# Kernel optimization log

Hardware: AMD Instinct MI355X
Metric: run time of the kernel (lower is better)

## Reference

```python
import jax, jax.numpy as jnp
import numpy as np

NUM_HEADS = 12

def setup_inputs() -> dict:
    key = jax.random.key(0)
    ks = jax.random.split(key, 9)
    B, N, C = 4, 1024, 768
    hd = C // NUM_HEADS  # 64
    return {
        "x": jax.random.normal(ks[0], (B, N, C), dtype=jnp.float32),
        "prev_attn": jax.random.uniform(ks[1], (B, NUM_HEADS, N, N), dtype=jnp.float32) / N,
        "qkv_w": jax.random.normal(ks[2], (3 * C, C), dtype=jnp.float32) * 0.02,
        "proj_w": jax.random.normal(ks[3], (C, C), dtype=jnp.float32) * 0.02,
        "proj_b": jax.random.normal(ks[4], (C,), dtype=jnp.float32) * 0.02,
        "bp_w1": jax.random.normal(ks[5], (hd // 2, 2 * hd), dtype=jnp.float32) * 0.02,
        "bp_b1": jax.random.normal(ks[6], (hd // 2,), dtype=jnp.float32) * 0.02,
        "bp_w2": jax.random.normal(ks[7], (3, hd // 2), dtype=jnp.float32) * 0.02,
        "bp_b2": jax.random.normal(ks[8], (3,), dtype=jnp.float32) * 0.02,
    }

def reference(x, prev_attn, qkv_w, proj_w, proj_b, bp_w1, bp_b1, bp_w2, bp_b2):
    B, N, C = x.shape
    H = NUM_HEADS
    hd = C // H
    scale = hd ** -0.5
    # qkv projection: [B,N,3C] -> [3,B,H,N,hd]
    qkv = (x @ qkv_w.T).reshape(B, N, 3, H, hd).transpose(2, 0, 3, 1, 4)
    q, k, v = qkv[0], qkv[1], qkv[2]
    # scaled dot-product scores [B,H,N,N]
    attn_logits = jnp.einsum('bhnd,bhmd->bhnm', q, k) * scale
    cur_attn = jax.nn.softmax(attn_logits, axis=-1)
    # per-(b,h,n) bias MLP on concat(q,k): [B,H,N,2*hd] -> [B,H,N,3]
    qk = jnp.concatenate((q, k), axis=-1)
    h1 = jax.nn.relu(jnp.einsum('bhnd,od->bhno', qk, bp_w1) + bp_b1)
    bias = jnp.abs(jnp.einsum('bhno,po->bhnp', h1, bp_w2) + bp_b2)  # [B,H,N,3]
    # blend current attention, previous attention, and uniform term
    attn = (cur_attn * (1.0 + bias[..., 0:1])
            + prev_attn * bias[..., 1:2]
            - bias[..., 2:3] / N)
    out = jnp.einsum('bhnm,bhmd->bhnd', attn, v)  # [B,H,N,hd]
    out = out.transpose(0, 2, 1, 3).reshape(B, N, C)
    out = out @ proj_w.T + proj_b
    return (out, cur_attn)
```

## Files before the change

### kernel.cpp

```cpp
#include <hip/hip_runtime.h>

typedef __bf16 bf16_t;
typedef __bf16 bf16x8 __attribute__((ext_vector_type(8)));
typedef __bf16 bf16x4 __attribute__((ext_vector_type(4)));
typedef float f32x4 __attribute__((ext_vector_type(4)));

static constexpr int Bb = 4, Hh = 12, Nn = 1024, Cc = 768, HD = 64;
static constexpr int OUT0 = Bb * Nn * Cc;

__global__ __launch_bounds__(256) void convert_all(
    const float* __restrict__ x, const float* __restrict__ qw, const float* __restrict__ pw,
    bf16_t* __restrict__ xb, bf16_t* __restrict__ qwb, bf16_t* __restrict__ pwb) {
  const int NX = (Bb * Nn * Cc) / 4;
  const int NQ = (3 * Cc * Cc) / 4;
  int i = blockIdx.x * 256 + threadIdx.x;
  const float4* src;
  bf16_t* dst;
  int off;
  if (i < NX) { src = (const float4*)x; dst = xb; off = i; }
  else if (i < NX + NQ) { src = (const float4*)qw; dst = qwb; off = i - NX; }
  else { src = (const float4*)pw; dst = pwb; off = i - NX - NQ; }
  float4 v = src[off];
  bf16x4 o;
  o[0] = (bf16_t)v.x; o[1] = (bf16_t)v.y; o[2] = (bf16_t)v.z; o[3] = (bf16_t)v.w;
  *(bf16x4*)(dst + (size_t)off * 4) = o;
}

template <int MODE>
__global__ __launch_bounds__(256) void gemm_bt(
    const bf16_t* __restrict__ A, const bf16_t* __restrict__ Bm, int N, int K,
    bf16_t* __restrict__ q_bf, bf16_t* __restrict__ k_bf, bf16_t* __restrict__ vT_bf,
    float* __restrict__ outF, const float* __restrict__ bias) {
  __shared__ bf16_t As[128 * 40];
  __shared__ bf16_t Bs[128 * 40];
  const int tid = threadIdx.x;
  const int lane = tid & 63;
  const int w = tid >> 6;
  const int wr = w >> 1, wc = w & 1;
  const int g = lane >> 4, r = lane & 15;
  const int ntiles = N >> 7;
  const int m0 = (blockIdx.x / ntiles) << 7;
  const int n0 = (blockIdx.x % ntiles) << 7;

  const f32x4 fz = {0.f, 0.f, 0.f, 0.f};
  f32x4 acc[4][4];
#pragma unroll
  for (int i = 0; i < 4; i++)
#pragma unroll
    for (int j = 0; j < 4; j++) acc[i][j] = fz;

  for (int k0 = 0; k0 < K; k0 += 32) {
#pragma unroll
    for (int p = 0; p < 2; p++) {
      int idx = tid + (p << 8);
      int row = idx >> 2;
      int kof = (idx & 3) << 3;
      *(bf16x8*)&As[row * 40 + kof] = *(const bf16x8*)&A[(size_t)(m0 + row) * K + k0 + kof];
      *(bf16x8*)&Bs[row * 40 + kof] = *(const bf16x8*)&Bm[(size_t)(n0 + row) * K + k0 + kof];
    }
    __syncthreads();
    bf16x8 af[4], bfv[4];
#pragma unroll
    for (int i = 0; i < 4; i++) af[i] = *(const bf16x8*)&As[(wr * 64 + i * 16 + r) * 40 + g * 8];
#pragma unroll
    for (int j = 0; j < 4; j++) bfv[j] = *(const bf16x8*)&Bs[(wc * 64 + j * 16 + r) * 40 + g * 8];
#pragma unroll
    for (int i = 0; i < 4; i++)
#pragma unroll
      for (int j = 0; j < 4; j++)
        acc[i][j] = __builtin_amdgcn_mfma_f32_16x16x32_bf16(af[i], bfv[j], acc[i][j], 0, 0, 0);
    __syncthreads();
  }

#pragma unroll
  for (int i = 0; i < 4; i++) {
#pragma unroll
    for (int j = 0; j < 4; j++) {
      int c = n0 + wc * 64 + j * 16 + r;
#pragma unroll
      for (int e = 0; e < 4; e++) {
        int mrow = m0 + wr * 64 + i * 16 + g * 4 + e;
        float val = acc[i][j][e];
        if constexpr (MODE == 0) {
          int which = c / 768;
          int cc = c - which * 768;
          int h = cc >> 6, d = cc & 63;
          int b = mrow >> 10, n = mrow & 1023;
          size_t bh = (size_t)(b * Hh + h);
          if (which == 0)      q_bf[(bh * Nn + n) * HD + d] = (bf16_t)val;
          else if (which == 1) k_bf[(bh * Nn + n) * HD + d] = (bf16_t)val;
          else                 vT_bf[(bh * HD + d) * Nn + n] = (bf16_t)val;
        } else {
          outF[(size_t)mrow * N + c] = val + bias[c];
        }
      }
    }
  }
}

__global__ __launch_bounds__(256) void bias_mlp(
    const bf16_t* __restrict__ qb, const bf16_t* __restrict__ kb,
    const float* __restrict__ w1, const float* __restrict__ b1,
    const float* __restrict__ w2, const float* __restrict__ b2,
    float* __restrict__ bias4) {
  __shared__ float w1s[32 * 129];
  __shared__ float qks[8][128];
  __shared__ float h1s[8][32];
  const int t = threadIdx.x;
#pragma unroll
  for (int p = 0; p < 16; p++) {
    int idx = p * 256 + t;
    w1s[(idx >> 7) * 129 + (idx & 127)] = w1[idx];
  }
  const int rl = t >> 5, u = t & 31;
  const int rowg = blockIdx.x * 8 + rl;
  {
    int i4 = u * 4;
    const bf16_t* src = (i4 < 64) ? (qb + (size_t)rowg * HD + i4)
                                  : (kb + (size_t)rowg * HD + (i4 - 64));
    bf16x4 vv = *(const bf16x4*)src;
#pragma unroll
    for (int z = 0; z < 4; z++) qks[rl][i4 + z] = (float)vv[z];
  }
  __syncthreads();
  float accv = b1[u];
#pragma unroll 8
  for (int i = 0; i < 128; i++) accv += qks[rl][i] * w1s[u * 129 + i];
  h1s[rl][u] = fmaxf(accv, 0.f);
  __syncthreads();
  if (u < 4) {
    float outv = 0.f;
    if (u < 3) {
      float s = b2[u];
#pragma unroll
      for (int j = 0; j < 32; j++) s += w2[u * 32 + j] * h1s[rl][j];
      float v = fabsf(s);
      outv = (u == 0) ? (1.f + v) : ((u == 1) ? v : -v * (1.f / (float)Nn));
    }
    bias4[(size_t)rowg * 4 + u] = outv;
  }
}

__global__ __launch_bounds__(256) void attn_fused(
    const bf16_t* __restrict__ qb, const bf16_t* __restrict__ kb,
    const bf16_t* __restrict__ vT, const float* __restrict__ prev,
    const float* __restrict__ bias4, float* __restrict__ cur,
    bf16_t* __restrict__ oh) {
  __shared__ bf16_t Pb[16 * 1024];
  __shared__ float redmax[16][4];
  __shared__ float redsum[16][4];
  const int bid = blockIdx.x;
  const int bh = bid >> 6, mt = bid & 63;
  const int tid = threadIdx.x;
  const int lane = tid & 63, w = tid >> 6;
  const int g = lane >> 4, r = lane & 15;
  const int row0 = mt << 4;

  const bf16_t* qp = qb + ((size_t)bh * Nn + row0) * HD;
  const bf16_t* kp = kb + (size_t)bh * Nn * HD;
  bf16x8 a0 = *(const bf16x8*)&qp[r * HD + g * 8];
  bf16x8 a1 = *(const bf16x8*)&qp[r * HD + g * 8 + 32];
  const f32x4 fz = {0.f, 0.f, 0.f, 0.f};
  f32x4 acc[16];
#pragma unroll
  for (int t = 0; t < 16; t++) {
    int col = (w << 8) + (t << 4) + r;
    bf16x8 b0 = *(const bf16x8*)&kp[(size_t)col * HD + g * 8];
    bf16x8 b1 = *(const bf16x8*)&kp[(size_t)col * HD + g * 8 + 32];
    f32x4 z = __builtin_amdgcn_mfma_f32_16x16x32_bf16(a0, b0, fz, 0, 0, 0);
    acc[t] = __builtin_amdgcn_mfma_f32_16x16x32_bf16(a1, b1, z, 0, 0, 0);
  }
  const float scale = 0.125f;
  float mj[4] = {-3.0e38f, -3.0e38f, -3.0e38f, -3.0e38f};
#pragma unroll
  for (int t = 0; t < 16; t++)
#pragma unroll
    for (int e = 0; e < 4; e++) {
      acc[t][e] *= scale;
      mj[e] = fmaxf(mj[e], acc[t][e]);
    }
#pragma unroll
  for (int s = 1; s < 16; s <<= 1)
#pragma unroll
    for (int e = 0; e < 4; e++) mj[e] = fmaxf(mj[e], __shfl_xor(mj[e], s, 64));
  if (r == 0) {
#pragma unroll
    for (int e = 0; e < 4; e++) redmax[g * 4 + e][w] = mj[e];
  }
  __syncthreads();
  float rm[4];
#pragma unroll
  for (int e = 0; e < 4; e++) {
    float v = fmaxf(redmax[g * 4 + e][0], redmax[g * 4 + e][1]);
    rm[e] = fmaxf(v, fmaxf(redmax[g * 4 + e][2], redmax[g * 4 + e][3]));
  }
  float sj[4] = {0.f, 0.f, 0.f, 0.f};
#pragma unroll
  for (int t = 0; t < 16; t++)
#pragma unroll
    for (int e = 0; e < 4; e++) {
      float ev = __expf(acc[t][e] - rm[e]);
      acc[t][e] = ev;
      sj[e] += ev;
    }
#pragma unroll
  for (int s = 1; s < 16; s <<= 1)
#pragma unroll
    for (int e = 0; e < 4; e++) sj[e] += __shfl_xor(sj[e], s, 64);
  if (r == 0) {
#pragma unroll
    for (int e = 0; e < 4; e++) redsum[g * 4 + e][w] = sj[e];
  }
  __syncthreads();
  float inv[4];
#pragma unroll
  for (int e = 0; e < 4; e++)
    inv[e] = 1.f / (redsum[g * 4 + e][0] + redsum[g * 4 + e][1] +
                    redsum[g * 4 + e][2] + redsum[g * 4 + e][3]);
  float* op = cur + (size_t)bh * Nn * Nn;
#pragma unroll
  for (int t = 0; t < 16; t++) {
    int col = (w << 8) + (t << 4) + r;
#pragma unroll
    for (int e = 0; e < 4; e++) {
      float p = acc[t][e] * inv[e];
      int row = g * 4 + e;
      op[(size_t)(row0 + row) * Nn + col] = p;
      Pb[row * 1024 + (col ^ ((row & 7) << 3))] = (bf16_t)p;
    }
  }
  __syncthreads();

  const float* pp = prev + (size_t)bh * Nn * Nn + (size_t)row0 * Nn;
  const float* bp = bias4 + ((size_t)(bh << 10) + row0) * 4;
#pragma unroll
  for (int i = 0; i < 16; i++) {
    float4 pv = *(const float4*)&pp[(size_t)i * Nn + tid * 4];
    float4 bv = *(const float4*)&bp[i * 4];
    int ci = (tid * 4) ^ ((i & 7) << 3);
    bf16x4 pbv = *(bf16x4*)&Pb[i * 1024 + ci];
    bf16x4 nb;
    nb[0] = (bf16_t)(bv.x * (float)pbv[0] + bv.y * pv.x + bv.z);
    nb[1] = (bf16_t)(bv.x * (float)pbv[1] + bv.y * pv.y + bv.z);
    nb[2] = (bf16_t)(bv.x * (float)pbv[2] + bv.y * pv.z + bv.z);
    nb[3] = (bf16_t)(bv.x * (float)pbv[3] + bv.y * pv.w + bv.z);
    *(bf16x4*)&Pb[i * 1024 + ci] = nb;
  }
  __syncthreads();

  const bf16_t* vp = vT + ((size_t)bh * HD + (w << 4) + r) * Nn;
  f32x4 c0 = fz, c1 = fz, c2 = fz, c3 = fz;
#pragma unroll
  for (int ks = 0; ks < 8; ks++) {
    int kA = ks * 32;
    bf16x8 afA = *(bf16x8*)&Pb[r * 1024 + ((kA + g * 8) ^ ((r & 7) << 3))];
    bf16x8 afB = *(bf16x8*)&Pb[r * 1024 + ((256 + kA + g * 8) ^ ((r & 7) << 3))];
    bf16x8 afC = *(bf16x8*)&Pb[r * 1024 + ((512 + kA + g * 8) ^ ((r & 7) << 3))];
    bf16x8 afD = *(bf16x8*)&Pb[r * 1024 + ((768 + kA + g * 8) ^ ((r & 7) << 3))];
    bf16x8 bA = *(const bf16x8*)&vp[kA + g * 8];
    bf16x8 bB = *(const bf16x8*)&vp[256 + kA + g * 8];
    bf16x8 bC = *(const bf16x8*)&vp[512 + kA + g * 8];
    bf16x8 bD = *(const bf16x8*)&vp[768 + kA + g * 8];
    c0 = __builtin_amdgcn_mfma_f32_16x16x32_bf16(afA, bA, c0, 0, 0, 0);
    c1 = __builtin_amdgcn_mfma_f32_16x16x32_bf16(afB, bB, c1, 0, 0, 0);
    c2 = __builtin_amdgcn_mfma_f32_16x16x32_bf16(afC, bC, c2, 0, 0, 0);
    c3 = __builtin_amdgcn_mfma_f32_16x16x32_bf16(afD, bD, c3, 0, 0, 0);
  }
  f32x4 osum = (c0 + c1) + (c2 + c3);
  const int b = bh / Hh, h = bh % Hh;
#pragma unroll
  for (int e = 0; e < 4; e++) {
    int nrow = row0 + g * 4 + e;
    oh[((size_t)(b * Nn + nrow)) * Cc + h * HD + (w << 4) + r] = (bf16_t)osum[e];
  }
}

extern "C" void kernel_launch(void* const* d_in, const int* in_sizes, int n_in,
                              void* d_out, int out_size, void* d_ws, size_t ws_size,
                              hipStream_t stream) {
  const float* x      = (const float*)d_in[0];
  const float* prev   = (const float*)d_in[1];
  const float* qkv_w  = (const float*)d_in[2];
  const float* proj_w = (const float*)d_in[3];
  const float* proj_b = (const float*)d_in[4];
  const float* bp_w1  = (const float*)d_in[5];
  const float* bp_b1  = (const float*)d_in[6];
  const float* bp_w2  = (const float*)d_in[7];
  const float* bp_w2b = (const float*)d_in[8];

  float* out0 = (float*)d_out;
  float* cur  = out0 + OUT0;

  char* ws = (char*)d_ws;
  bf16_t* xb    = (bf16_t*)(ws + 0);
  bf16_t* qwb   = (bf16_t*)(ws + 6291456);
  bf16_t* pwb   = (bf16_t*)(ws + 9830400);
  bf16_t* qbf   = (bf16_t*)(ws + 11010048);
  bf16_t* kbf   = (bf16_t*)(ws + 17301504);
  bf16_t* vtb   = (bf16_t*)(ws + 23592960);
  float*  bias4 = (float*)(ws + 29884416);
  bf16_t* ohb   = (bf16_t*)(ws + 30670848);
  if (ws_size < 36962304) return;

  convert_all<<<5376, 256, 0, stream>>>(x, qkv_w, proj_w, xb, qwb, pwb);
  gemm_bt<0><<<(4096 / 128) * (2304 / 128), 256, 0, stream>>>(
      xb, qwb, 2304, 768, qbf, kbf, vtb, nullptr, nullptr);
  bias_mlp<<<49152 / 8, 256, 0, stream>>>(qbf, kbf, bp_w1, bp_b1, bp_w2, bp_w2b, bias4);
  attn_fused<<<48 * 64, 256, 0, stream>>>(qbf, kbf, vtb, prev, bias4, cur, ohb);
  gemm_bt<1><<<(4096 / 128) * (768 / 128), 256, 0, stream>>>(
      ohb, pwb, 768, 768, nullptr, nullptr, nullptr, out0, proj_b);
}
```

Measured before the change: 249.1 us.

## Widen attention block to 512 threads and stage fp32 probabilities in LDS for coalesced writes

```diff
diff --git a/kernel.cpp b/kernel.cpp
--- a/kernel.cpp
+++ b/kernel.cpp
@@ -141,14 +141,16 @@
   }
 }
 
-__global__ __launch_bounds__(256) void attn_fused(
+__global__ __launch_bounds__(512, 4) void attn_fused(
     const bf16_t* __restrict__ qb, const bf16_t* __restrict__ kb,
     const bf16_t* __restrict__ vT, const float* __restrict__ prev,
     const float* __restrict__ bias4, float* __restrict__ cur,
     bf16_t* __restrict__ oh) {
-  __shared__ bf16_t Pb[16 * 1024];
-  __shared__ float redmax[16][4];
-  __shared__ float redsum[16][4];
+  __shared__ float Pf[16 * 1024];
+  __shared__ float redmax[16][8];
+  __shared__ float redsum[16][8];
+  bf16_t* Pb = (bf16_t*)Pf;
+  f32x4* Ppart = (f32x4*)(Pf + 8192);
   const int bid = blockIdx.x;
   const int bh = bid >> 6, mt = bid & 63;
   const int tid = threadIdx.x;
@@ -161,10 +163,10 @@
   bf16x8 a0 = *(const bf16x8*)&qp[r * HD + g * 8];
   bf16x8 a1 = *(const bf16x8*)&qp[r * HD + g * 8 + 32];
   const f32x4 fz = {0.f, 0.f, 0.f, 0.f};
-  f32x4 acc[16];
-#pragma unroll
-  for (int t = 0; t < 16; t++) {
-    int col = (w << 8) + (t << 4) + r;
+  f32x4 acc[8];
+#pragma unroll
+  for (int t = 0; t < 8; t++) {
+    int col = (w << 7) + (t << 4) + r;
     bf16x8 b0 = *(const bf16x8*)&kp[(size_t)col * HD + g * 8];
     bf16x8 b1 = *(const bf16x8*)&kp[(size_t)col * HD + g * 8 + 32];
     f32x4 z = __builtin_amdgcn_mfma_f32_16x16x32_bf16(a0, b0, fz, 0, 0, 0);
@@ -173,7 +175,7 @@
   const float scale = 0.125f;
   float mj[4] = {-3.0e38f, -3.0e38f, -3.0e38f, -3.0e38f};
 #pragma unroll
-  for (int t = 0; t < 16; t++)
+  for (int t = 0; t < 8; t++)
 #pragma unroll
     for (int e = 0; e < 4; e++) {
       acc[t][e] *= scale;
@@ -191,12 +193,14 @@
   float rm[4];
 #pragma unroll
   for (int e = 0; e < 4; e++) {
-    float v = fmaxf(redmax[g * 4 + e][0], redmax[g * 4 + e][1]);
-    rm[e] = fmaxf(v, fmaxf(redmax[g * 4 + e][2], redmax[g * 4 + e][3]));
+    float v = redmax[g * 4 + e][0];
+#pragma unroll
+    for (int q = 1; q < 8; q++) v = fmaxf(v, redmax[g * 4 + e][q]);
+    rm[e] = v;
   }
   float sj[4] = {0.f, 0.f, 0.f, 0.f};
 #pragma unroll
-  for (int t = 0; t < 16; t++)
+  for (int t = 0; t < 8; t++)
 #pragma unroll
     for (int e = 0; e < 4; e++) {
       float ev = __expf(acc[t][e] - rm[e]);
@@ -214,64 +218,77 @@
   __syncthreads();
   float inv[4];
 #pragma unroll
-  for (int e = 0; e < 4; e++)
-    inv[e] = 1.f / (redsum[g * 4 + e][0] + redsum[g * 4 + e][1] +
-                    redsum[g * 4 + e][2] + redsum[g * 4 + e][3]);
-  float* op = cur + (size_t)bh * Nn * Nn;
-#pragma unroll
-  for (int t = 0; t < 16; t++) {
-    int col = (w << 8) + (t << 4) + r;
+  for (int e = 0; e < 4; e++) {
+    float v = redsum[g * 4 + e][0];
+#pragma unroll
+    for (int q = 1; q < 8; q++) v += redsum[g * 4 + e][q];
+    inv[e] = 1.f / v;
+  }
+#pragma unroll
+  for (int t = 0; t < 8; t++) {
+    int col = (w << 7) + (t << 4) + r;
 #pragma unroll
     for (int e = 0; e < 4; e++) {
-      float p = acc[t][e] * inv[e];
       int row = g * 4 + e;
-      op[(size_t)(row0 + row) * Nn + col] = p;
-      Pb[row * 1024 + (col ^ ((row & 7) << 3))] = (bf16_t)p;
-    }
-  }
-  __syncthreads();
-
-  const float* pp = prev + (size_t)bh * Nn * Nn + (size_t)row0 * Nn;
-  const float* bp = bias4 + ((size_t)(bh << 10) + row0) * 4;
-#pragma unroll
-  for (int i = 0; i < 16; i++) {
-    float4 pv = *(const float4*)&pp[(size_t)i * Nn + tid * 4];
+      Pf[row * 1024 + (col ^ ((g & 1) << 4))] = acc[t][e] * inv[e];
+    }
+  }
+  __syncthreads();
+
+  const int half = tid >> 8;
+  const int c = (tid & 255) << 2;
+  const float* pp = prev + (size_t)bh * Nn * Nn + (size_t)(row0 + half * 8) * Nn + c;
+  float* cp = cur + (size_t)bh * Nn * Nn + (size_t)(row0 + half * 8) * Nn + c;
+  const float* bp = bias4 + ((size_t)(bh << 10) + row0 + half * 8) * 4;
+  float4 pv[8];
+#pragma unroll
+  for (int i = 0; i < 8; i++) pv[i] = *(const float4*)&pp[(size_t)i * Nn];
+  bf16x4 pbreg[8];
+#pragma unroll
+  for (int i = 0; i < 8; i++) {
+    int row = half * 8 + i;
+    int sw = ((row >> 2) & 1) << 4;
+    float4 pf = *(const float4*)&Pf[row * 1024 + (c ^ sw)];
+    *(float4*)&cp[(size_t)i * Nn] = pf;
     float4 bv = *(const float4*)&bp[i * 4];
-    int ci = (tid * 4) ^ ((i & 7) << 3);
-    bf16x4 pbv = *(bf16x4*)&Pb[i * 1024 + ci];
-    bf16x4 nb;
-    nb[0] = (bf16_t)(bv.x * (float)pbv[0] + bv.y * pv.x + bv.z);
-    nb[1] = (bf16_t)(bv.x * (float)pbv[1] + bv.y * pv.y + bv.z);
-    nb[2] = (bf16_t)(bv.x * (float)pbv[2] + bv.y * pv.z + bv.z);
-    nb[3] = (bf16_t)(bv.x * (float)pbv[3] + bv.y * pv.w + bv.z);
-    *(bf16x4*)&Pb[i * 1024 + ci] = nb;
-  }
-  __syncthreads();
-
-  const bf16_t* vp = vT + ((size_t)bh * HD + (w << 4) + r) * Nn;
-  f32x4 c0 = fz, c1 = fz, c2 = fz, c3 = fz;
+    pbreg[i][0] = (bf16_t)(bv.x * pf.x + bv.y * pv[i].x + bv.z);
+    pbreg[i][1] = (bf16_t)(bv.x * pf.y + bv.y * pv[i].y + bv.z);
+    pbreg[i][2] = (bf16_t)(bv.x * pf.z + bv.y * pv[i].z + bv.z);
+    pbreg[i][3] = (bf16_t)(bv.x * pf.w + bv.y * pv[i].w + bv.z);
+  }
+  __syncthreads();
+#pragma unroll
+  for (int i = 0; i < 8; i++) {
+    int row = half * 8 + i;
+    *(bf16x4*)&Pb[row * 1024 + (c ^ ((row & 7) << 3))] = pbreg[i];
+  }
+  __syncthreads();
+
+  const int cg = w & 3, kh = w >> 2;
+  const bf16_t* vp = vT + ((size_t)bh * HD + (cg << 4) + r) * Nn + (kh << 9);
+  f32x4 c0 = fz, c1 = fz;
 #pragma unroll
   for (int ks = 0; ks < 8; ks++) {
-    int kA = ks * 32;
-    bf16x8 afA = *(bf16x8*)&Pb[r * 1024 + ((kA + g * 8) ^ ((r & 7) << 3))];
-    bf16x8 afB = *(bf16x8*)&Pb[r * 1024 + ((256 + kA + g * 8) ^ ((r & 7) << 3))];
-    bf16x8 afC = *(bf16x8*)&Pb[r * 1024 + ((512 + kA + g * 8) ^ ((r & 7) << 3))];
-    bf16x8 afD = *(bf16x8*)&Pb[r * 1024 + ((768 + kA + g * 8) ^ ((r & 7) << 3))];
-    bf16x8 bA = *(const bf16x8*)&vp[kA + g * 8];
-    bf16x8 bB = *(const bf16x8*)&vp[256 + kA + g * 8];
-    bf16x8 bC = *(const bf16x8*)&vp[512 + kA + g * 8];
-    bf16x8 bD = *(const bf16x8*)&vp[768 + kA + g * 8];
+    int kA = ks * 32 + g * 8;
+    int k0 = (kh << 9) + kA;
+    bf16x8 afA = *(bf16x8*)&Pb[r * 1024 + (k0 ^ ((r & 7) << 3))];
+    bf16x8 afB = *(bf16x8*)&Pb[r * 1024 + ((k0 + 256) ^ ((r & 7) << 3))];
+    bf16x8 bA = *(const bf16x8*)&vp[kA];
+    bf16x8 bB = *(const bf16x8*)&vp[256 + kA];
     c0 = __builtin_amdgcn_mfma_f32_16x16x32_bf16(afA, bA, c0, 0, 0, 0);
     c1 = __builtin_amdgcn_mfma_f32_16x16x32_bf16(afB, bB, c1, 0, 0, 0);
-    c2 = __builtin_amdgcn_mfma_f32_16x16x32_bf16(afC, bC, c2, 0, 0, 0);
-    c3 = __builtin_amdgcn_mfma_f32_16x16x32_bf16(afD, bD, c3, 0, 0, 0);
-  }
-  f32x4 osum = (c0 + c1) + (c2 + c3);
-  const int b = bh / Hh, h = bh % Hh;
-#pragma unroll
-  for (int e = 0; e < 4; e++) {
-    int nrow = row0 + g * 4 + e;
-    oh[((size_t)(b * Nn + nrow)) * Cc + h * HD + (w << 4) + r] = (bf16_t)osum[e];
+  }
+  f32x4 part = c0 + c1;
+  if (kh == 1) Ppart[cg * 64 + lane] = part;
+  __syncthreads();
+  if (kh == 0) {
+    f32x4 tot = part + Ppart[cg * 64 + lane];
+    const int b = bh / Hh, h = bh % Hh;
+#pragma unroll
+    for (int e = 0; e < 4; e++) {
+      int nrow = row0 + g * 4 + e;
+      oh[((size_t)(b * Nn + nrow)) * Cc + h * HD + (cg << 4) + r] = (bf16_t)tot[e];
+    }
   }
 }
 
@@ -306,7 +323,7 @@
   gemm_bt<0><<<(4096 / 128) * (2304 / 128), 256, 0, stream>>>(
       xb, qwb, 2304, 768, qbf, kbf, vtb, nullptr, nullptr);
   bias_mlp<<<49152 / 8, 256, 0, stream>>>(qbf, kbf, bp_w1, bp_b1, bp_w2, bp_w2b, bias4);
-  attn_fused<<<48 * 64, 256, 0, stream>>>(qbf, kbf, vtb, prev, bias4, cur, ohb);
+  attn_fused<<<48 * 64, 512, 0, stream>>>(qbf, kbf, vtb, prev, bias4, cur, ohb);
   gemm_bt<1><<<(4096 / 128) * (768 / 128), 256, 0, stream>>>(
       ohb, pwb, 768, 768, nullptr, nullptr, nullptr, out0, proj_b);
 }
```

After: 256.4 us. +2.9%, slower.

## Restructure attention into single-wave two-pass streaming softmax with recomputed QK

Applied to the files above, without the earlier changes.

```diff
diff --git a/kernel.cpp b/kernel.cpp
--- a/kernel.cpp
+++ b/kernel.cpp
@@ -141,138 +141,144 @@
   }
 }
 
-__global__ __launch_bounds__(256) void attn_fused(
+__global__ __launch_bounds__(64, 3) void attn_fused(
     const bf16_t* __restrict__ qb, const bf16_t* __restrict__ kb,
     const bf16_t* __restrict__ vT, const float* __restrict__ prev,
     const float* __restrict__ bias4, float* __restrict__ cur,
     bf16_t* __restrict__ oh) {
-  __shared__ bf16_t Pb[16 * 1024];
-  __shared__ float redmax[16][4];
-  __shared__ float redsum[16][4];
+  __shared__ float P_lds[16 * 68];
+  __shared__ bf16_t Pbs[16 * 64];
+  __shared__ float biasr[16 * 4];
   const int bid = blockIdx.x;
   const int bh = bid >> 6, mt = bid & 63;
-  const int tid = threadIdx.x;
-  const int lane = tid & 63, w = tid >> 6;
+  const int lane = threadIdx.x & 63;
   const int g = lane >> 4, r = lane & 15;
   const int row0 = mt << 4;
+  const float scale = 0.125f;
 
   const bf16_t* qp = qb + ((size_t)bh * Nn + row0) * HD;
   const bf16_t* kp = kb + (size_t)bh * Nn * HD;
   bf16x8 a0 = *(const bf16x8*)&qp[r * HD + g * 8];
   bf16x8 a1 = *(const bf16x8*)&qp[r * HD + g * 8 + 32];
+
+  if (lane < 16)
+    *(float4*)&biasr[lane * 4] =
+        *(const float4*)&bias4[((size_t)(bh << 10) + row0 + lane) * 4];
+
   const f32x4 fz = {0.f, 0.f, 0.f, 0.f};
-  f32x4 acc[16];
-#pragma unroll
+  float m_[4] = {-3.0e38f, -3.0e38f, -3.0e38f, -3.0e38f};
+  float s_[4] = {0.f, 0.f, 0.f, 0.f};
+
   for (int t = 0; t < 16; t++) {
-    int col = (w << 8) + (t << 4) + r;
-    bf16x8 b0 = *(const bf16x8*)&kp[(size_t)col * HD + g * 8];
-    bf16x8 b1 = *(const bf16x8*)&kp[(size_t)col * HD + g * 8 + 32];
-    f32x4 z = __builtin_amdgcn_mfma_f32_16x16x32_bf16(a0, b0, fz, 0, 0, 0);
-    acc[t] = __builtin_amdgcn_mfma_f32_16x16x32_bf16(a1, b1, z, 0, 0, 0);
-  }
-  const float scale = 0.125f;
-  float mj[4] = {-3.0e38f, -3.0e38f, -3.0e38f, -3.0e38f};
-#pragma unroll
-  for (int t = 0; t < 16; t++)
+    const int c0 = t << 6;
+    f32x4 l[4];
+#pragma unroll
+    for (int sub = 0; sub < 4; sub++) {
+      const bf16_t* kr = &kp[(size_t)(c0 + (sub << 4) + r) * HD + g * 8];
+      bf16x8 b0 = *(const bf16x8*)kr;
+      bf16x8 b1 = *(const bf16x8*)(kr + 32);
+      f32x4 z = __builtin_amdgcn_mfma_f32_16x16x32_bf16(a0, b0, fz, 0, 0, 0);
+      l[sub] = __builtin_amdgcn_mfma_f32_16x16x32_bf16(a1, b1, z, 0, 0, 0);
+    }
+    float tm[4];
 #pragma unroll
     for (int e = 0; e < 4; e++) {
-      acc[t][e] *= scale;
-      mj[e] = fmaxf(mj[e], acc[t][e]);
-    }
-#pragma unroll
-  for (int s = 1; s < 16; s <<= 1)
-#pragma unroll
-    for (int e = 0; e < 4; e++) mj[e] = fmaxf(mj[e], __shfl_xor(mj[e], s, 64));
-  if (r == 0) {
-#pragma unroll
-    for (int e = 0; e < 4; e++) redmax[g * 4 + e][w] = mj[e];
-  }
-  __syncthreads();
-  float rm[4];
-#pragma unroll
-  for (int e = 0; e < 4; e++) {
-    float v = fmaxf(redmax[g * 4 + e][0], redmax[g * 4 + e][1]);
-    rm[e] = fmaxf(v, fmaxf(redmax[g * 4 + e][2], redmax[g * 4 + e][3]));
-  }
-  float sj[4] = {0.f, 0.f, 0.f, 0.f};
-#pragma unroll
-  for (int t = 0; t < 16; t++)
+      float v0 = fmaxf(l[0][e], l[1][e]);
+      float v1 = fmaxf(l[2][e], l[3][e]);
+      tm[e] = fmaxf(v0, v1) * scale;
+    }
+#pragma unroll
+    for (int sh = 1; sh < 16; sh <<= 1)
+#pragma unroll
+      for (int e = 0; e < 4; e++) tm[e] = fmaxf(tm[e], __shfl_xor(tm[e], sh, 64));
+    float ts[4];
 #pragma unroll
     for (int e = 0; e < 4; e++) {
-      float ev = __expf(acc[t][e] - rm[e]);
-      acc[t][e] = ev;
-      sj[e] += ev;
-    }
-#pragma unroll
-  for (int s = 1; s < 16; s <<= 1)
-#pragma unroll
-    for (int e = 0; e < 4; e++) sj[e] += __shfl_xor(sj[e], s, 64);
-  if (r == 0) {
-#pragma unroll
-    for (int e = 0; e < 4; e++) redsum[g * 4 + e][w] = sj[e];
-  }
-  __syncthreads();
+      float nm = fmaxf(m_[e], tm[e]);
+      float f = __expf(m_[e] - nm);
+      float sum = __expf(l[0][e] * scale - nm) + __expf(l[1][e] * scale - nm) +
+                  __expf(l[2][e] * scale - nm) + __expf(l[3][e] * scale - nm);
+      ts[e] = sum;
+      m_[e] = nm;
+      s_[e] = s_[e] * f;
+    }
+#pragma unroll
+    for (int sh = 1; sh < 16; sh <<= 1)
+#pragma unroll
+      for (int e = 0; e < 4; e++) ts[e] += __shfl_xor(ts[e], sh, 64);
+#pragma unroll
+    for (int e = 0; e < 4; e++) s_[e] += ts[e];
+  }
   float inv[4];
 #pragma unroll
-  for (int e = 0; e < 4; e++)
-    inv[e] = 1.f / (redsum[g * 4 + e][0] + redsum[g * 4 + e][1] +
-                    redsum[g * 4 + e][2] + redsum[g * 4 + e][3]);
-  float* op = cur + (size_t)bh * Nn * Nn;
-#pragma unroll
+  for (int e = 0; e < 4; e++) inv[e] = 1.f / s_[e];
+
+  asm volatile("s_waitcnt lgkmcnt(0)" ::: "memory");
+  f32x4 oacc[4] = {fz, fz, fz, fz};
+  const float* pp = prev + (size_t)bh * Nn * Nn + (size_t)row0 * Nn;
+  float* cp = cur + (size_t)bh * Nn * Nn + (size_t)row0 * Nn;
+  const bf16_t* vp = vT + (size_t)bh * HD * Nn;
+
   for (int t = 0; t < 16; t++) {
-    int col = (w << 8) + (t << 4) + r;
+    const int c0 = t << 6;
+    f32x4 l[4];
+#pragma unroll
+    for (int sub = 0; sub < 4; sub++) {
+      const bf16_t* kr = &kp[(size_t)(c0 + (sub << 4) + r) * HD + g * 8];
+      bf16x8 b0 = *(const bf16x8*)kr;
+      bf16x8 b1 = *(const bf16x8*)(kr + 32);
+      f32x4 z = __builtin_amdgcn_mfma_f32_16x16x32_bf16(a0, b0, fz, 0, 0, 0);
+      l[sub] = __builtin_amdgcn_mfma_f32_16x16x32_bf16(a1, b1, z, 0, 0, 0);
+    }
+#pragma unroll
+    for (int sub = 0; sub < 4; sub++)
+#pragma unroll
+      for (int e = 0; e < 4; e++) {
+        float p = __expf(l[sub][e] * scale - m_[e]) * inv[e];
+        P_lds[(g * 4 + e) * 68 + (sub << 4) + r] = p;
+      }
+    asm volatile("s_waitcnt lgkmcnt(0)" ::: "memory");
+    __builtin_amdgcn_wave_barrier();
+#pragma unroll
+    for (int i = 0; i < 4; i++) {
+      int row = (i << 2) + g;
+      int col4 = r << 2;
+      float4 pf = *(float4*)&P_lds[row * 68 + col4];
+      float4 pv = *(const float4*)&pp[(size_t)row * Nn + c0 + col4];
+      *(float4*)&cp[(size_t)row * Nn + c0 + col4] = pf;
+      float4 bv = *(float4*)&biasr[row * 4];
+      bf16x4 pb;
+      pb[0] = (bf16_t)(bv.x * pf.x + bv.y * pv.x + bv.z);
+      pb[1] = (bf16_t)(bv.x * pf.y + bv.y * pv.y + bv.z);
+      pb[2] = (bf16_t)(bv.x * pf.z + bv.y * pv.z + bv.z);
+      pb[3] = (bf16_t)(bv.x * pf.w + bv.y * pv.w + bv.z);
+      int byteoff = ((row << 7) + (col4 << 1)) ^ ((row & 7) << 4);
+      *(bf16x4*)((char*)Pbs + byteoff) = pb;
+    }
+    asm volatile("s_waitcnt lgkmcnt(0)" ::: "memory");
+    __builtin_amdgcn_wave_barrier();
+    bf16x8 pa0 = *(bf16x8*)((char*)Pbs + (((r << 7) + (g << 4)) ^ ((r & 7) << 4)));
+    bf16x8 pa1 = *(bf16x8*)((char*)Pbs + (((r << 7) + 64 + (g << 4)) ^ ((r & 7) << 4)));
+#pragma unroll
+    for (int d0 = 0; d0 < 4; d0++) {
+      const bf16_t* vr = &vp[(size_t)((d0 << 4) + r) * Nn + c0 + g * 8];
+      bf16x8 vb0 = *(const bf16x8*)vr;
+      bf16x8 vb1 = *(const bf16x8*)(vr + 32);
+      oacc[d0] = __builtin_amdgcn_mfma_f32_16x16x32_bf16(pa0, vb0, oacc[d0], 0, 0, 0);
+      oacc[d0] = __builtin_amdgcn_mfma_f32_16x16x32_bf16(pa1, vb1, oacc[d0], 0, 0, 0);
+    }
+    asm volatile("s_waitcnt lgkmcnt(0)" ::: "memory");
+    __builtin_amdgcn_wave_barrier();
+  }
+
+  const int b = bh / Hh, h = bh % Hh;
+#pragma unroll
+  for (int d0 = 0; d0 < 4; d0++)
 #pragma unroll
     for (int e = 0; e < 4; e++) {
-      float p = acc[t][e] * inv[e];
-      int row = g * 4 + e;
-      op[(size_t)(row0 + row) * Nn + col] = p;
-      Pb[row * 1024 + (col ^ ((row & 7) << 3))] = (bf16_t)p;
-    }
-  }
-  __syncthreads();
-
-  const float* pp = prev + (size_t)bh * Nn * Nn + (size_t)row0 * Nn;
-  const float* bp = bias4 + ((size_t)(bh << 10) + row0) * 4;
-#pragma unroll
-  for (int i = 0; i < 16; i++) {
-    float4 pv = *(const float4*)&pp[(size_t)i * Nn + tid * 4];
-    float4 bv = *(const float4*)&bp[i * 4];
-    int ci = (tid * 4) ^ ((i & 7) << 3);
-    bf16x4 pbv = *(bf16x4*)&Pb[i * 1024 + ci];
-    bf16x4 nb;
-    nb[0] = (bf16_t)(bv.x * (float)pbv[0] + bv.y * pv.x + bv.z);
-    nb[1] = (bf16_t)(bv.x * (float)pbv[1] + bv.y * pv.y + bv.z);
-    nb[2] = (bf16_t)(bv.x * (float)pbv[2] + bv.y * pv.z + bv.z);
-    nb[3] = (bf16_t)(bv.x * (float)pbv[3] + bv.y * pv.w + bv.z);
-    *(bf16x4*)&Pb[i * 1024 + ci] = nb;
-  }
-  __syncthreads();
-
-  const bf16_t* vp = vT + ((size_t)bh * HD + (w << 4) + r) * Nn;
-  f32x4 c0 = fz, c1 = fz, c2 = fz, c3 = fz;
-#pragma unroll
-  for (int ks = 0; ks < 8; ks++) {
-    int kA = ks * 32;
-    bf16x8 afA = *(bf16x8*)&Pb[r * 1024 + ((kA + g * 8) ^ ((r & 7) << 3))];
-    bf16x8 afB = *(bf16x8*)&Pb[r * 1024 + ((256 + kA + g * 8) ^ ((r & 7) << 3))];
-    bf16x8 afC = *(bf16x8*)&Pb[r * 1024 + ((512 + kA + g * 8) ^ ((r & 7) << 3))];
-    bf16x8 afD = *(bf16x8*)&Pb[r * 1024 + ((768 + kA + g * 8) ^ ((r & 7) << 3))];
-    bf16x8 bA = *(const bf16x8*)&vp[kA + g * 8];
-    bf16x8 bB = *(const bf16x8*)&vp[256 + kA + g * 8];
-    bf16x8 bC = *(const bf16x8*)&vp[512 + kA + g * 8];
-    bf16x8 bD = *(const bf16x8*)&vp[768 + kA + g * 8];
-    c0 = __builtin_amdgcn_mfma_f32_16x16x32_bf16(afA, bA, c0, 0, 0, 0);
-    c1 = __builtin_amdgcn_mfma_f32_16x16x32_bf16(afB, bB, c1, 0, 0, 0);
-    c2 = __builtin_amdgcn_mfma_f32_16x16x32_bf16(afC, bC, c2, 0, 0, 0);
-    c3 = __builtin_amdgcn_mfma_f32_16x16x32_bf16(afD, bD, c3, 0, 0, 0);
-  }
-  f32x4 osum = (c0 + c1) + (c2 + c3);
-  const int b = bh / Hh, h = bh % Hh;
-#pragma unroll
-  for (int e = 0; e < 4; e++) {
-    int nrow = row0 + g * 4 + e;
-    oh[((size_t)(b * Nn + nrow)) * Cc + h * HD + (w << 4) + r] = (bf16_t)osum[e];
-  }
+      int nrow = row0 + g * 4 + e;
+      oh[((size_t)(b * Nn + nrow)) * Cc + h * HD + (d0 << 4) + r] = (bf16_t)oacc[d0][e];
+    }
 }
 
 extern "C" void kernel_launch(void* const* d_in, const int* in_sizes, int n_in,
@@ -306,7 +312,7 @@
   gemm_bt<0><<<(4096 / 128) * (2304 / 128), 256, 0, stream>>>(
       xb, qwb, 2304, 768, qbf, kbf, vtb, nullptr, nullptr);
   bias_mlp<<<49152 / 8, 256, 0, stream>>>(qbf, kbf, bp_w1, bp_b1, bp_w2, bp_w2b, bias4);
-  attn_fused<<<48 * 64, 256, 0, stream>>>(qbf, kbf, vtb, prev, bias4, cur, ohb);
+  attn_fused<<<48 * 64, 64, 0, stream>>>(qbf, kbf, vtb, prev, bias4, cur, ohb);
   gemm_bt<1><<<(4096 / 128) * (768 / 128), 256, 0, stream>>>(
       ohb, pwb, 768, 768, nullptr, nullptr, nullptr, out0, proj_b);
 }
```

Measured after the change: 285.6 us. 1.15x slower.
